# Performance work log

Measured on AMD Instinct MI355X. Metric: run time of the kernel, lower is better.

Reference implementation:

```python
import jax, jax.numpy as jnp
import numpy as np

SCALE = 0.125          # feature stride 8
OUT = 7                # roi_align output size
SR = 2                 # sampling_ratio
BBW = (10.0, 10.0, 5.0, 5.0)   # torchvision BoxCoder weights
CLAMP = float(np.log(1000.0 / 16.0))
IMG_H, IMG_W = 800.0, 1088.0


def _bilinear(img, ys, xs):
    # img [C,H,W]; ys,xs [P] -> [C,P]
    C, H, W = img.shape
    y = jnp.clip(ys, 0.0, H - 1.0)
    x = jnp.clip(xs, 0.0, W - 1.0)
    y0 = jnp.floor(y); x0 = jnp.floor(x)
    y0i = y0.astype(jnp.int32); x0i = x0.astype(jnp.int32)
    y1i = jnp.minimum(y0i + 1, H - 1); x1i = jnp.minimum(x0i + 1, W - 1)
    ly = y - y0; lx = x - x0
    flat = img.reshape(C, H * W)
    g = lambda yi, xi: flat[:, yi * W + xi]
    return (g(y0i, x0i) * (1 - ly) * (1 - lx) + g(y0i, x1i) * (1 - ly) * lx
            + g(y1i, x0i) * ly * (1 - lx) + g(y1i, x1i) * ly * lx)


def _roi_align(features, boxes, roi_batch):
    # features [B,C,H,W], boxes [N,4] (image coords), roi_batch [N] -> [N,C,7,7]
    B, C, H, W = features.shape
    P = OUT * SR

    def one(b, box):
        x1, y1, x2, y2 = box[0] * SCALE, box[1] * SCALE, box[2] * SCALE, box[3] * SCALE
        rw = jnp.maximum(x2 - x1, 1.0)
        rh = jnp.maximum(y2 - y1, 1.0)
        bw = rw / OUT; bh = rh / OUT
        off = (jnp.arange(OUT)[:, None] + (jnp.arange(SR)[None, :] + 0.5) / SR).reshape(-1)  # [P]
        ys = y1 + off * bh
        xs = x1 + off * bw
        yy = jnp.repeat(ys, P)   # [P*P], y-major
        xx = jnp.tile(xs, P)
        v = _bilinear(features[b], yy, xx)                   # [C, P*P]
        return v.reshape(C, OUT, SR, OUT, SR).mean(axis=(2, 4))  # avg over samples

    return jax.vmap(one)(roi_batch, boxes)


def _decode(deltas, boxes):
    # deltas [N,K,4], boxes [N,4] -> [N,K,4]
    pw = boxes[:, 2] - boxes[:, 0]
    ph = boxes[:, 3] - boxes[:, 1]
    cx = boxes[:, 0] + 0.5 * pw
    cy = boxes[:, 1] + 0.5 * ph
    dx = deltas[..., 0] / BBW[0]; dy = deltas[..., 1] / BBW[1]
    dw = jnp.minimum(deltas[..., 2] / BBW[2], CLAMP)
    dh = jnp.minimum(deltas[..., 3] / BBW[3], CLAMP)
    pcx = dx * pw[:, None] + cx[:, None]
    pcy = dy * ph[:, None] + cy[:, None]
    pww = jnp.exp(dw) * pw[:, None]
    phh = jnp.exp(dh) * ph[:, None]
    out = jnp.stack([
        jnp.clip(pcx - 0.5 * pww, 0.0, IMG_W),
        jnp.clip(pcy - 0.5 * phh, 0.0, IMG_H),
        jnp.clip(pcx + 0.5 * pww, 0.0, IMG_W),
        jnp.clip(pcy + 0.5 * phh, 0.0, IMG_H),
    ], axis=-1)
    return out


def setup_inputs() -> dict:
    key = jax.random.key(0)
    ks = jax.random.split(key, 12)
    B, C, H, W, N, NC = 2, 256, 100, 136, 1000, 2
    features = jax.random.normal(ks[0], (B, C, H, W), jnp.float32)
    # valid proposal boxes in image coords
    cx = jax.random.uniform(ks[1], (N,)) * IMG_W
    cy = jax.random.uniform(ks[2], (N,)) * IMG_H
    bw = jax.random.uniform(ks[3], (N,)) * 240.0 + 16.0
    bh = jax.random.uniform(ks[4], (N,)) * 240.0 + 16.0
    x1 = jnp.clip(cx - 0.5 * bw, 0.0, IMG_W - 2.0)
    y1 = jnp.clip(cy - 0.5 * bh, 0.0, IMG_H - 2.0)
    x2 = jnp.clip(x1 + bw, x1 + 1.0, IMG_W - 1.0)
    y2 = jnp.clip(y1 + bh, y1 + 1.0, IMG_H - 1.0)
    boxes = jnp.stack([x1, y1, x2, y2], axis=-1).astype(jnp.float32)
    roi_batch = jax.random.randint(ks[5], (N,), 0, B, dtype=jnp.int32)
    D = C * OUT * OUT  # 12544
    HID = 1024
    s = 0.02
    fc1_w = jax.random.normal(ks[6], (D, HID), jnp.float32) * s
    fc1_b = jnp.zeros((HID,), jnp.float32)
    fc2_w = jax.random.normal(ks[7], (HID, HID), jnp.float32) * s
    fc2_b = jnp.zeros((HID,), jnp.float32)
    cls_w = jax.random.normal(ks[8], (HID, NC), jnp.float32) * s
    cls_b = jnp.zeros((NC,), jnp.float32)
    bbox_w = jax.random.normal(ks[9], (HID, NC * 4), jnp.float32) * s
    bbox_b = jnp.zeros((NC * 4,), jnp.float32)
    return {"features": features, "boxes": boxes, "roi_batch": roi_batch,
            "fc1_w": fc1_w, "fc1_b": fc1_b, "fc2_w": fc2_w, "fc2_b": fc2_b,
            "cls_w": cls_w, "cls_b": cls_b, "bbox_w": bbox_w, "bbox_b": bbox_b}


def reference(features, boxes, roi_batch, fc1_w, fc1_b, fc2_w, fc2_b, cls_w, cls_b, bbox_w, bbox_b):
    N = boxes.shape[0]
    feats = _roi_align(features, boxes, roi_batch).reshape(N, -1)  # [N, 12544]
    h = jax.nn.relu(feats @ fc1_w + fc1_b)                         # TwoMLPHead fc6
    h = jax.nn.relu(h @ fc2_w + fc2_b)                             # TwoMLPHead fc7
    scores = jax.nn.softmax(h @ cls_w + cls_b, axis=-1)            # [N, 2]
    deltas = (h @ bbox_w + bbox_b).reshape(N, -1, 4)               # [N, 2, 4]
    dec = _decode(deltas, boxes).reshape(N, -1)                    # [N, 8]
    return jnp.concatenate([dec, scores], axis=-1)                 # [N, 10]
```

## Files before the change

kernel.cpp:

```cpp
#include <hip/hip_runtime.h>
#include <hip/hip_bf16.h>

#define BF16 __hip_bfloat16

typedef __bf16 bf16x8 __attribute__((ext_vector_type(8)));
typedef float floatx4 __attribute__((ext_vector_type(4)));
typedef int intx4 __attribute__((ext_vector_type(4)));

__global__ __launch_bounds__(256) void transpose_all(const float* __restrict__ features,
                                                     const float* __restrict__ fc1_w,
                                                     const float* __restrict__ fc2_w,
                                                     BF16* __restrict__ featT,
                                                     BF16* __restrict__ w1t,
                                                     BF16* __restrict__ w2t) {
    __shared__ float tile[32][33];
    int bid = blockIdx.x;
    const float* ip;
    BF16* op;
    int R, C, cx, cy;
    if (bid < 6800) {
        int z = bid / 3400, r = bid - z * 3400;
        cx = r % 425; cy = r / 425;
        R = 256; C = 13600;
        ip = features + (size_t)z * 256 * 13600;
        op = featT + (size_t)z * 256 * 13600;
    } else if (bid < 19344) {
        int r = bid - 6800;
        cx = r & 31; cy = r >> 5;
        R = 12544; C = 1024;
        ip = fc1_w; op = w1t;
    } else {
        int r = bid - 19344;
        cx = r & 31; cy = r >> 5;
        R = 1024; C = 1024;
        ip = fc2_w; op = w2t;
    }
    int tx = threadIdx.x & 31, ty = threadIdx.x >> 5;
    int r0 = cy << 5, c0 = cx << 5;
#pragma unroll
    for (int i = 0; i < 4; ++i)
        tile[ty + i * 8][tx] = ip[(size_t)(r0 + ty + i * 8) * C + c0 + tx];
    __syncthreads();
#pragma unroll
    for (int i = 0; i < 4; ++i)
        op[(size_t)(c0 + ty + i * 8) * R + r0 + tx] = __float2bfloat16(tile[tx][ty + i * 8]);
}

__global__ __launch_bounds__(256) void roi_align_k(const BF16* __restrict__ featT,
                                                   const float* __restrict__ boxes,
                                                   const int* __restrict__ roi_batch,
                                                   BF16* __restrict__ feats) {
    __shared__ __align__(16) int   s_off[196][4];
    __shared__ __align__(16) float s_w[196][4];
    __shared__ BF16 lbuf[12544];
    int roi = blockIdx.x;
    int t = threadIdx.x;
    BF16* orow = feats + (size_t)roi * 12544;
    if (roi >= 1000) {
        uint4* o4 = (uint4*)orow;
        uint4 z = {0u, 0u, 0u, 0u};
        for (int i = t; i < 1568; i += 256) o4[i] = z;
        return;
    }
    int b = roi_batch[roi];

    if (t < 196) {
        float x1 = boxes[roi * 4 + 0] * 0.125f;
        float y1 = boxes[roi * 4 + 1] * 0.125f;
        float x2 = boxes[roi * 4 + 2] * 0.125f;
        float y2 = boxes[roi * 4 + 3] * 0.125f;
        float bw = fmaxf(x2 - x1, 1.0f) * (1.0f / 7.0f);
        float bh = fmaxf(y2 - y1, 1.0f) * (1.0f / 7.0f);
        int cell = t >> 2, s = t & 3;
        int oy = cell / 7, ox = cell - oy * 7;
        int sy = s >> 1, sx = s & 1;
        float yc = y1 + ((float)oy + ((float)sy + 0.5f) * 0.5f) * bh;
        float xc = x1 + ((float)ox + ((float)sx + 0.5f) * 0.5f) * bw;
        yc = fminf(fmaxf(yc, 0.0f), 99.0f);
        xc = fminf(fmaxf(xc, 0.0f), 135.0f);
        float y0f = floorf(yc), x0f = floorf(xc);
        int y0 = (int)y0f, x0 = (int)x0f;
        int y1i = min(y0 + 1, 99), x1i = min(x0 + 1, 135);
        float ly = yc - y0f, lx = xc - x0f;
        s_w[t][0] = (1.0f - ly) * (1.0f - lx) * 0.25f;
        s_w[t][1] = (1.0f - ly) * lx * 0.25f;
        s_w[t][2] = ly * (1.0f - lx) * 0.25f;
        s_w[t][3] = ly * lx * 0.25f;
        s_off[t][0] = (y0 * 136 + x0) * 256;
        s_off[t][1] = (y0 * 136 + x1i) * 256;
        s_off[t][2] = (y1i * 136 + x0) * 256;
        s_off[t][3] = (y1i * 136 + x1i) * 256;
    }
    __syncthreads();

    int cb = t & 31, g = t >> 5;
    const BF16* fb = featT + (size_t)b * (100 * 136 * 256) + cb * 8;
    int chbase = cb * 8;
    for (int cell = g; cell < 49; cell += 8) {
        float a[8];
#pragma unroll
        for (int j = 0; j < 8; ++j) a[j] = 0.0f;
#pragma unroll
        for (int s = 0; s < 4; ++s) {
            int p = cell * 4 + s;
#pragma unroll
            for (int tap = 0; tap < 4; ++tap) {
                float w = s_w[p][tap];
                bf16x8 v = *(const bf16x8*)(fb + s_off[p][tap]);
#pragma unroll
                for (int j = 0; j < 8; ++j) a[j] += w * (float)v[j];
            }
        }
#pragma unroll
        for (int j = 0; j < 8; ++j)
            lbuf[(chbase + j) * 49 + cell] = __float2bfloat16(a[j]);
    }
    __syncthreads();
    uint4* o4 = (uint4*)orow;
    const uint4* l4 = (const uint4*)lbuf;
    for (int i = t; i < 1568; i += 256) o4[i] = l4[i];
}

__global__ __launch_bounds__(256) void gemm_splitk(const BF16* __restrict__ A,
                                                   const BF16* __restrict__ Bt,
                                                   float* __restrict__ P,
                                                   int K, int chunk) {
    __shared__ char lds[2][2][16384];
    int w = threadIdx.x >> 6, l = threadIdx.x & 63;
    int wm = w & 1, wn = w >> 1;
    int lin = blockIdx.x;
    int tn = lin & 7;
    int tm = (lin >> 3) & 7;
    int s  = lin >> 6;
    int k0 = s * chunk;

    floatx4 acc[4][4];
#pragma unroll
    for (int i = 0; i < 4; ++i)
#pragma unroll
        for (int j = 0; j < 4; ++j) acc[i][j] = (floatx4){0.f, 0.f, 0.f, 0.f};

    const size_t strideA = (size_t)K * 2;
    int r8 = l >> 3;
    int g8 = (l & 7) ^ r8;
    const char* gA = (const char*)A + (size_t)(tm * 128 + w * 32 + r8) * strideA
                     + (size_t)k0 * 2 + (size_t)g8 * 16;
    const char* gB = (const char*)Bt + (size_t)(tn * 128 + w * 32 + r8) * strideA
                     + (size_t)k0 * 2 + (size_t)g8 * 16;
    int lw = w * 4096 + l * 16;

    int c = l & 15, q = l >> 4;
    int xa0 = ((0 * 4 + q) ^ (c & 7)) * 16;
    int xa1 = ((1 * 4 + q) ^ (c & 7)) * 16;
    int abase = (wm * 64 + c) * 128;
    int bbase = (wn * 64 + c) * 128;

    int nIter = chunk >> 6;

    intx4 pa[4], pb[4];
#pragma unroll
    for (int i = 0; i < 4; ++i) {
        pa[i] = *(const intx4*)(gA + (size_t)(i * 8) * strideA);
        pb[i] = *(const intx4*)(gB + (size_t)(i * 8) * strideA);
    }
#pragma unroll
    for (int i = 0; i < 4; ++i) {
        *(intx4*)(&lds[0][0][lw + i * 1024]) = pa[i];
        *(intx4*)(&lds[0][1][lw + i * 1024]) = pb[i];
    }
    __syncthreads();

    for (int kb = 0; kb < nIter; ++kb) {
        int cur = kb & 1;
        bool more = (kb + 1 < nIter);
        if (more) {
            size_t ko = (size_t)(kb + 1) * 128;
#pragma unroll
            for (int i = 0; i < 4; ++i) {
                pa[i] = *(const intx4*)(gA + (size_t)(i * 8) * strideA + ko);
                pb[i] = *(const intx4*)(gB + (size_t)(i * 8) * strideA + ko);
            }
        }
        const char* bufA = lds[cur][0];
        const char* bufB = lds[cur][1];
#pragma unroll
        for (int kk = 0; kk < 2; ++kk) {
            int xo = kk ? xa1 : xa0;
            bf16x8 af[4], bfr[4];
#pragma unroll
            for (int mi = 0; mi < 4; ++mi) af[mi] = *(const bf16x8*)(bufA + abase + mi * 2048 + xo);
#pragma unroll
            for (int ni = 0; ni < 4; ++ni) bfr[ni] = *(const bf16x8*)(bufB + bbase + ni * 2048 + xo);
#pragma unroll
            for (int mi = 0; mi < 4; ++mi)
#pragma unroll
                for (int ni = 0; ni < 4; ++ni)
                    acc[mi][ni] = __builtin_amdgcn_mfma_f32_16x16x32_bf16(af[mi], bfr[ni], acc[mi][ni], 0, 0, 0);
        }
        if (more) {
            char* nA = &lds[cur ^ 1][0][lw];
            char* nB = &lds[cur ^ 1][1][lw];
#pragma unroll
            for (int i = 0; i < 4; ++i) {
                *(intx4*)(nA + i * 1024) = pa[i];
                *(intx4*)(nB + i * 1024) = pb[i];
            }
        }
        __syncthreads();
    }

    size_t base = (size_t)s << 20;
#pragma unroll
    for (int mi = 0; mi < 4; ++mi) {
        int rowG = tm * 128 + wm * 64 + mi * 16 + q * 4;
#pragma unroll
        for (int ni = 0; ni < 4; ++ni) {
            int colG = tn * 128 + wn * 64 + ni * 16 + c;
#pragma unroll
            for (int r = 0; r < 4; ++r)
                P[base + (size_t)(rowG + r) * 1024 + colG] = acc[mi][ni][r];
        }
    }
}

__global__ __launch_bounds__(256) void reduce_k(const float* __restrict__ P,
                                                const float* __restrict__ bias,
                                                BF16* __restrict__ out,
                                                int S) {
    int i = blockIdx.x * 256 + threadIdx.x;
    float a = bias[i & 1023];
    for (int s = 0; s < S; ++s) a += P[((size_t)s << 20) + i];
    a = fmaxf(a, 0.0f);
    out[i] = __float2bfloat16(a);
}

__global__ __launch_bounds__(256) void head_k(const float* __restrict__ P2,
                                              const float* __restrict__ fc2_b,
                                              const float* __restrict__ cls_w,
                                              const float* __restrict__ cls_b,
                                              const float* __restrict__ bbox_w,
                                              const float* __restrict__ bbox_b,
                                              const float* __restrict__ boxes,
                                              float* __restrict__ out, int S2) {
    __shared__ float red[4][10];
    int roi = blockIdx.x;
    int t = threadIdx.x, w = t >> 6, l = t & 63;
    int k4 = t * 4;

    floatx4 h = *(const floatx4*)(fc2_b + k4);
    const float* pbase = P2 + (size_t)roi * 1024 + k4;
    for (int s = 0; s < S2; ++s) {
        floatx4 p = *(const floatx4*)(pbase + ((size_t)s << 20));
        h.x += p.x; h.y += p.y; h.z += p.z; h.w += p.w;
    }
    h.x = fmaxf(h.x, 0.f); h.y = fmaxf(h.y, 0.f); h.z = fmaxf(h.z, 0.f); h.w = fmaxf(h.w, 0.f);

    float acc[10];
#pragma unroll
    for (int j = 0; j < 10; ++j) acc[j] = 0.0f;
    floatx4 c0 = *(const floatx4*)(cls_w + k4 * 2);
    floatx4 c1 = *(const floatx4*)(cls_w + k4 * 2 + 4);
    acc[0] = h.x * c0.x + h.y * c0.z + h.z * c1.x + h.w * c1.z;
    acc[1] = h.x * c0.y + h.y * c0.w + h.z * c1.y + h.w * c1.w;
    const float* bw = bbox_w + k4 * 8;
#pragma unroll
    for (int kk = 0; kk < 4; ++kk) {
        float hv = (kk == 0) ? h.x : (kk == 1) ? h.y : (kk == 2) ? h.z : h.w;
        floatx4 b0 = *(const floatx4*)(bw + kk * 8);
        floatx4 b1 = *(const floatx4*)(bw + kk * 8 + 4);
        acc[2] += hv * b0.x; acc[3] += hv * b0.y; acc[4] += hv * b0.z; acc[5] += hv * b0.w;
        acc[6] += hv * b1.x; acc[7] += hv * b1.y; acc[8] += hv * b1.z; acc[9] += hv * b1.w;
    }
#pragma unroll
    for (int j = 0; j < 10; ++j) {
#pragma unroll
        for (int off = 32; off > 0; off >>= 1) acc[j] += __shfl_down(acc[j], off);
    }
    if (l == 0) {
#pragma unroll
        for (int j = 0; j < 10; ++j) red[w][j] = acc[j];
    }
    __syncthreads();
    if (t == 0) {
        float f[10];
#pragma unroll
        for (int j = 0; j < 10; ++j) f[j] = red[0][j] + red[1][j] + red[2][j] + red[3][j];
        float s0 = f[0] + cls_b[0], s1 = f[1] + cls_b[1];
        float m = fmaxf(s0, s1);
        float e0 = expf(s0 - m), e1 = expf(s1 - m);
        float inv = 1.0f / (e0 + e1);

        float bx1 = boxes[roi * 4 + 0], by1 = boxes[roi * 4 + 1];
        float bx2 = boxes[roi * 4 + 2], by2 = boxes[roi * 4 + 3];
        float pw = bx2 - bx1, ph = by2 - by1;
        float cx = bx1 + 0.5f * pw, cy = by1 + 0.5f * ph;
        const float CLAMPV = 4.135166556742356f;
        float* orow = out + roi * 10;
#pragma unroll
        for (int cl = 0; cl < 2; ++cl) {
            float dx = (f[2 + cl * 4 + 0] + bbox_b[cl * 4 + 0]) * 0.1f;
            float dy = (f[2 + cl * 4 + 1] + bbox_b[cl * 4 + 1]) * 0.1f;
            float dw = fminf((f[2 + cl * 4 + 2] + bbox_b[cl * 4 + 2]) * 0.2f, CLAMPV);
            float dh = fminf((f[2 + cl * 4 + 3] + bbox_b[cl * 4 + 3]) * 0.2f, CLAMPV);
            float pcx = dx * pw + cx, pcy = dy * ph + cy;
            float pww = expf(dw) * pw, phh = expf(dh) * ph;
            orow[cl * 4 + 0] = fminf(fmaxf(pcx - 0.5f * pww, 0.0f), 1088.0f);
            orow[cl * 4 + 1] = fminf(fmaxf(pcy - 0.5f * phh, 0.0f), 800.0f);
            orow[cl * 4 + 2] = fminf(fmaxf(pcx + 0.5f * pww, 0.0f), 1088.0f);
            orow[cl * 4 + 3] = fminf(fmaxf(pcy + 0.5f * phh, 0.0f), 800.0f);
        }
        orow[8] = e0 * inv;
        orow[9] = e1 * inv;
    }
}

extern "C" void kernel_launch(void* const* d_in, const int* in_sizes, int n_in,
                              void* d_out, int out_size, void* d_ws, size_t ws_size,
                              hipStream_t stream) {
    const float* features = (const float*)d_in[0];
    const float* boxes    = (const float*)d_in[1];
    const int*   roi_b    = (const int*)d_in[2];
    const float* fc1_w    = (const float*)d_in[3];
    const float* fc1_b    = (const float*)d_in[4];
    const float* fc2_w    = (const float*)d_in[5];
    const float* fc2_b    = (const float*)d_in[6];
    const float* cls_w    = (const float*)d_in[7];
    const float* cls_b    = (const float*)d_in[8];
    const float* bbox_w   = (const float*)d_in[9];
    const float* bbox_b   = (const float*)d_in[10];
    float* out = (float*)d_out;

    char* ws = (char*)d_ws;
    BF16* featT = (BF16*)(ws + 0);
    BF16* w1t   = (BF16*)(ws + 13926400);
    BF16* w2t   = (BF16*)(ws + 39616512);
    BF16* feats = (BF16*)(ws + 41713664);
    BF16* h1    = (BF16*)(ws + 67403776);
    float* P1   = (float*)(ws + 69500928);
    float* P2   = (float*)(ws + 0);

    int S1 = 7;
    int S2 = 4;

    transpose_all<<<20368, 256, 0, stream>>>(features, fc1_w, fc2_w, featT, w1t, w2t);

    roi_align_k<<<1024, 256, 0, stream>>>(featT, boxes, roi_b, feats);

    gemm_splitk<<<64 * S1, 256, 0, stream>>>(feats, w1t, P1, 12544, 12544 / S1);
    reduce_k<<<4096, 256, 0, stream>>>(P1, fc1_b, h1, S1);

    gemm_splitk<<<64 * S2, 256, 0, stream>>>(h1, w2t, P2, 1024, 1024 / S2);

    head_k<<<1000, 256, 0, stream>>>(P2, fc2_b, cls_w, cls_b, bbox_w, bbox_b, boxes, out, S2);
}
```

Baseline: 216.8 us.

## Overlap weight transposes with ROI align and deepen GEMM global prefetch

The fc1/fc2 weight transposes move out of the first transpose kernel and into the ROI-align launch as extra blocks. Those blocks reuse the ROI kernel's LDS buffer as the transpose tile, so the weight conversion can run alongside ROI sampling instead of in front of it. The split-K GEMM main loop is unrolled by two with two register sets, so global loads are issued two K-steps ahead of the MFMA work. The costs are higher register pressure in the GEMM, and transpose blocks now carry the ROI kernel's larger LDS footprint, which can lower occupancy for them.

```diff
diff --git a/kernel.cpp b/kernel.cpp
--- a/kernel.cpp
+++ b/kernel.cpp
@@ -7,34 +7,15 @@
 typedef float floatx4 __attribute__((ext_vector_type(4)));
 typedef int intx4 __attribute__((ext_vector_type(4)));
 
-__global__ __launch_bounds__(256) void transpose_all(const float* __restrict__ features,
-                                                     const float* __restrict__ fc1_w,
-                                                     const float* __restrict__ fc2_w,
-                                                     BF16* __restrict__ featT,
-                                                     BF16* __restrict__ w1t,
-                                                     BF16* __restrict__ w2t) {
+__global__ __launch_bounds__(256) void transpose_feat(const float* __restrict__ features,
+                                                      BF16* __restrict__ featT) {
     __shared__ float tile[32][33];
     int bid = blockIdx.x;
-    const float* ip;
-    BF16* op;
-    int R, C, cx, cy;
-    if (bid < 6800) {
-        int z = bid / 3400, r = bid - z * 3400;
-        cx = r % 425; cy = r / 425;
-        R = 256; C = 13600;
-        ip = features + (size_t)z * 256 * 13600;
-        op = featT + (size_t)z * 256 * 13600;
-    } else if (bid < 19344) {
-        int r = bid - 6800;
-        cx = r & 31; cy = r >> 5;
-        R = 12544; C = 1024;
-        ip = fc1_w; op = w1t;
-    } else {
-        int r = bid - 19344;
-        cx = r & 31; cy = r >> 5;
-        R = 1024; C = 1024;
-        ip = fc2_w; op = w2t;
-    }
+    int z = bid / 3400, r = bid - z * 3400;
+    int cx = r % 425, cy = r / 425;
+    const int R = 256, C = 13600;
+    const float* ip = features + (size_t)z * R * C;
+    BF16* op = featT + (size_t)z * R * C;
     int tx = threadIdx.x & 31, ty = threadIdx.x >> 5;
     int r0 = cy << 5, c0 = cx << 5;
 #pragma unroll
@@ -46,15 +27,49 @@
         op[(size_t)(c0 + ty + i * 8) * R + r0 + tx] = __float2bfloat16(tile[tx][ty + i * 8]);
 }
 
-__global__ __launch_bounds__(256) void roi_align_k(const BF16* __restrict__ featT,
-                                                   const float* __restrict__ boxes,
-                                                   const int* __restrict__ roi_batch,
-                                                   BF16* __restrict__ feats) {
+__global__ __launch_bounds__(256) void roi_and_wt(const BF16* __restrict__ featT,
+                                                  const float* __restrict__ boxes,
+                                                  const int* __restrict__ roi_batch,
+                                                  BF16* __restrict__ feats,
+                                                  const float* __restrict__ fc1_w,
+                                                  const float* __restrict__ fc2_w,
+                                                  BF16* __restrict__ w1t,
+                                                  BF16* __restrict__ w2t) {
     __shared__ __align__(16) int   s_off[196][4];
     __shared__ __align__(16) float s_w[196][4];
     __shared__ BF16 lbuf[12544];
-    int roi = blockIdx.x;
+    int bid = blockIdx.x;
     int t = threadIdx.x;
+
+    if (bid >= 1024) {
+        float (*tile)[33] = (float (*)[33])lbuf;
+        int r = bid - 1024;
+        const float* ip;
+        BF16* op;
+        int R, C, cx, cy;
+        if (r < 12544) {
+            cx = r & 31; cy = r >> 5;
+            R = 12544; C = 1024;
+            ip = fc1_w; op = w1t;
+        } else {
+            int r2 = r - 12544;
+            cx = r2 & 31; cy = r2 >> 5;
+            R = 1024; C = 1024;
+            ip = fc2_w; op = w2t;
+        }
+        int tx = t & 31, ty = t >> 5;
+        int r0 = cy << 5, c0 = cx << 5;
+#pragma unroll
+        for (int i = 0; i < 4; ++i)
+            tile[ty + i * 8][tx] = ip[(size_t)(r0 + ty + i * 8) * C + c0 + tx];
+        __syncthreads();
+#pragma unroll
+        for (int i = 0; i < 4; ++i)
+            op[(size_t)(c0 + ty + i * 8) * R + r0 + tx] = __float2bfloat16(tile[tx][ty + i * 8]);
+        return;
+    }
+
+    int roi = bid;
     BF16* orow = feats + (size_t)roi * 12544;
     if (roi >= 1000) {
         uint4* o4 = (uint4*)orow;
@@ -157,57 +172,84 @@
 
     int nIter = chunk >> 6;
 
-    intx4 pa[4], pb[4];
+    intx4 ra[4], rb[4], sa[4], sb[4];
 #pragma unroll
     for (int i = 0; i < 4; ++i) {
-        pa[i] = *(const intx4*)(gA + (size_t)(i * 8) * strideA);
-        pb[i] = *(const intx4*)(gB + (size_t)(i * 8) * strideA);
+        ra[i] = *(const intx4*)(gA + (size_t)(i * 8) * strideA);
+        rb[i] = *(const intx4*)(gB + (size_t)(i * 8) * strideA);
+    }
+    if (nIter > 1) {
+#pragma unroll
+        for (int i = 0; i < 4; ++i) {
+            sa[i] = *(const intx4*)(gA + (size_t)(i * 8) * strideA + 128);
+            sb[i] = *(const intx4*)(gB + (size_t)(i * 8) * strideA + 128);
+        }
     }
 #pragma unroll
     for (int i = 0; i < 4; ++i) {
-        *(intx4*)(&lds[0][0][lw + i * 1024]) = pa[i];
-        *(intx4*)(&lds[0][1][lw + i * 1024]) = pb[i];
-    }
-    __syncthreads();
-
-    for (int kb = 0; kb < nIter; ++kb) {
-        int cur = kb & 1;
-        bool more = (kb + 1 < nIter);
-        if (more) {
-            size_t ko = (size_t)(kb + 1) * 128;
+        *(intx4*)(&lds[0][0][lw + i * 1024]) = ra[i];
+        *(intx4*)(&lds[0][1][lw + i * 1024]) = rb[i];
+    }
+    __syncthreads();
+
+#define MFMA_STEP(BUF)                                                                  \
+    {                                                                                   \
+        const char* bufA = lds[BUF][0];                                                 \
+        const char* bufB = lds[BUF][1];                                                 \
+        _Pragma("unroll")                                                               \
+        for (int kk = 0; kk < 2; ++kk) {                                                \
+            int xo = kk ? xa1 : xa0;                                                    \
+            bf16x8 af[4], bfr[4];                                                       \
+            _Pragma("unroll")                                                           \
+            for (int mi = 0; mi < 4; ++mi) af[mi] = *(const bf16x8*)(bufA + abase + mi * 2048 + xo); \
+            _Pragma("unroll")                                                           \
+            for (int ni = 0; ni < 4; ++ni) bfr[ni] = *(const bf16x8*)(bufB + bbase + ni * 2048 + xo); \
+            _Pragma("unroll")                                                           \
+            for (int mi = 0; mi < 4; ++mi)                                              \
+                _Pragma("unroll")                                                       \
+                for (int ni = 0; ni < 4; ++ni)                                          \
+                    acc[mi][ni] = __builtin_amdgcn_mfma_f32_16x16x32_bf16(af[mi], bfr[ni], acc[mi][ni], 0, 0, 0); \
+        }                                                                               \
+    }
+
+    for (int kb = 0; kb < nIter; kb += 2) {
+        if (kb + 2 < nIter) {
+            size_t ko = (size_t)(kb + 2) * 128;
 #pragma unroll
             for (int i = 0; i < 4; ++i) {
-                pa[i] = *(const intx4*)(gA + (size_t)(i * 8) * strideA + ko);
-                pb[i] = *(const intx4*)(gB + (size_t)(i * 8) * strideA + ko);
-            }
-        }
-        const char* bufA = lds[cur][0];
-        const char* bufB = lds[cur][1];
-#pragma unroll
-        for (int kk = 0; kk < 2; ++kk) {
-            int xo = kk ? xa1 : xa0;
-            bf16x8 af[4], bfr[4];
-#pragma unroll
-            for (int mi = 0; mi < 4; ++mi) af[mi] = *(const bf16x8*)(bufA + abase + mi * 2048 + xo);
-#pragma unroll
-            for (int ni = 0; ni < 4; ++ni) bfr[ni] = *(const bf16x8*)(bufB + bbase + ni * 2048 + xo);
-#pragma unroll
-            for (int mi = 0; mi < 4; ++mi)
-#pragma unroll
-                for (int ni = 0; ni < 4; ++ni)
-                    acc[mi][ni] = __builtin_amdgcn_mfma_f32_16x16x32_bf16(af[mi], bfr[ni], acc[mi][ni], 0, 0, 0);
-        }
-        if (more) {
-            char* nA = &lds[cur ^ 1][0][lw];
-            char* nB = &lds[cur ^ 1][1][lw];
+                ra[i] = *(const intx4*)(gA + (size_t)(i * 8) * strideA + ko);
+                rb[i] = *(const intx4*)(gB + (size_t)(i * 8) * strideA + ko);
+            }
+        }
+        MFMA_STEP(0)
+        if (kb + 1 < nIter) {
 #pragma unroll
             for (int i = 0; i < 4; ++i) {
-                *(intx4*)(nA + i * 1024) = pa[i];
-                *(intx4*)(nB + i * 1024) = pb[i];
+                *(intx4*)(&lds[1][0][lw + i * 1024]) = sa[i];
+                *(intx4*)(&lds[1][1][lw + i * 1024]) = sb[i];
             }
         }
         __syncthreads();
-    }
+        if (kb + 1 >= nIter) break;
+        if (kb + 3 < nIter) {
+            size_t ko = (size_t)(kb + 3) * 128;
+#pragma unroll
+            for (int i = 0; i < 4; ++i) {
+                sa[i] = *(const intx4*)(gA + (size_t)(i * 8) * strideA + ko);
+                sb[i] = *(const intx4*)(gB + (size_t)(i * 8) * strideA + ko);
+            }
+        }
+        MFMA_STEP(1)
+        if (kb + 2 < nIter) {
+#pragma unroll
+            for (int i = 0; i < 4; ++i) {
+                *(intx4*)(&lds[0][0][lw + i * 1024]) = ra[i];
+                *(intx4*)(&lds[0][1][lw + i * 1024]) = rb[i];
+            }
+        }
+        __syncthreads();
+    }
+#undef MFMA_STEP
 
     size_t base = (size_t)s << 20;
 #pragma unroll
@@ -342,9 +384,10 @@
     int S1 = 7;
     int S2 = 4;
 
-    transpose_all<<<20368, 256, 0, stream>>>(features, fc1_w, fc2_w, featT, w1t, w2t);
-
-    roi_align_k<<<1024, 256, 0, stream>>>(featT, boxes, roi_b, feats);
+    transpose_feat<<<6800, 256, 0, stream>>>(features, featT);
+
+    roi_and_wt<<<1024 + 12544 + 1024, 256, 0, stream>>>(featT, boxes, roi_b, feats,
+                                                        fc1_w, fc2_w, w1t, w2t);
 
     gemm_splitk<<<64 * S1, 256, 0, stream>>>(feats, w1t, P1, 12544, 12544 / S1);
     reduce_k<<<4096, 256, 0, stream>>>(P1, fc1_b, h1, S1);
```

Measured after the change: 236.1 us. 8.9% more time.
